# Kernel optimization log

Measured on AMD Instinct MI355X. Metric: run time of the kernel, lower is better.

Reference implementation:

```python
import jax, jax.numpy as jnp
import numpy as np

N_NODES = 20000
N_EDGES = 640000
D = 128


def setup_inputs() -> dict:
    key = jax.random.key(0)
    ks = jax.random.split(key, 8)
    scale = 1.0 / np.sqrt(D)
    x = jax.random.normal(ks[0], (N_NODES, D), dtype=jnp.float32)
    edge_index = jax.random.randint(ks[1], (2, N_EDGES), 0, N_NODES, dtype=jnp.int64)
    W1_rel = jax.random.normal(ks[2], (D, D), dtype=jnp.float32) * scale
    b1_rel = jnp.zeros((D,), dtype=jnp.float32)
    W1_root = jax.random.normal(ks[3], (D, D), dtype=jnp.float32) * scale
    W2_rel = jax.random.normal(ks[4], (D, D), dtype=jnp.float32) * scale
    b2_rel = jnp.zeros((D,), dtype=jnp.float32)
    W2_root = jax.random.normal(ks[5], (D, D), dtype=jnp.float32) * scale
    return {"x": x, "edge_index": edge_index,
            "W1_rel": W1_rel, "b1_rel": b1_rel, "W1_root": W1_root,
            "W2_rel": W2_rel, "b2_rel": b2_rel, "W2_root": W2_root}


def _graph_conv(x, src, dst, W_rel, b_rel, W_root):
    # sum-aggregate neighbor features: gather from src, scatter-add to dst
    agg = jax.ops.segment_sum(x[src], dst, num_segments=N_NODES)  # [N, D]
    # PyG GraphConv: lin_rel(agg) (with bias) + lin_root(x) (no bias)
    return agg @ W_rel + b_rel + x @ W_root


def reference(x, edge_index, W1_rel, b1_rel, W1_root, W2_rel, b2_rel, W2_root):
    src, dst = edge_index[0], edge_index[1]  # messages flow src (j) -> dst (i)
    h = jax.nn.relu(_graph_conv(x, src, dst, W1_rel, b1_rel, W1_root))
    out = _graph_conv(h, src, dst, W2_rel, b2_rel, W2_root)  # final ReLU stripped
    return out
```

## Files before the change

### kernel.cpp

```cpp
#include <hip/hip_runtime.h>

#define N_NODES 20000
#define N_EDGES 640000
#define D 128
#define CAP 128
#define NBINS 157
#define PA_BLOCKS 256
#define EPB 2500
#define SLABCAP 40
#define SRC_SPLIT 10000

typedef __attribute__((ext_vector_type(8))) short bf16x8;
typedef __attribute__((ext_vector_type(4))) float f32x4;

__device__ __forceinline__ short f2bf(float f) {
    union { float f; unsigned u; } un; un.f = f;
    unsigned r = un.u + 0x7fff + ((un.u >> 16) & 1);
    return (short)(r >> 16);
}
__device__ __forceinline__ float bflo(unsigned u) { return __uint_as_float(u << 16); }
__device__ __forceinline__ float bfhi(unsigned u) { return __uint_as_float(u & 0xffff0000u); }

__global__ __launch_bounds__(256) void prep_kernel(
    const float* __restrict__ x,
    const int* __restrict__ src, const int* __restrict__ dst,
    const float* __restrict__ W1_rel, const float* __restrict__ W1_root,
    const float* __restrict__ W2_rel, const float* __restrict__ W2_root,
    unsigned* __restrict__ binned, int* __restrict__ cnts,
    short* __restrict__ xb, short* __restrict__ wpk1, short* __restrict__ wpk2)
{
    const int b = blockIdx.x;
    const int tid = threadIdx.x;
    if (b < PA_BLOCKS) {
        __shared__ int sOff[NBINS];
        for (int i = tid; i < NBINS; i += 256) sOff[i] = 0;
        __syncthreads();
        const int e0 = b * EPB;
        for (int idx = tid; idx < EPB; idx += 256) {
            int d = dst[e0 + idx];
            int s = src[e0 + idx];
            int bin = d >> 7;
            int off = atomicAdd(&sOff[bin], 1);
            if (off < SLABCAP)
                binned[(size_t)(bin * PA_BLOCKS + b) * SLABCAP + off] =
                    ((unsigned)(d & 127) << 16) | (unsigned)s;
        }
        __syncthreads();
        for (int i = tid; i < NBINS; i += 256) {
            int c = sOff[i];
            cnts[i * PA_BLOCKS + b] = (c > SLABCAP) ? SLABCAP : c;
        }
    } else if (b < PA_BLOCKS + 2500) {
        int i = (b - PA_BLOCKS) * 256 + tid;
        float4 v = ((const float4*)x)[i];
        ushort4 o;
        o.x = (unsigned short)f2bf(v.x);
        o.y = (unsigned short)f2bf(v.y);
        o.z = (unsigned short)f2bf(v.z);
        o.w = (unsigned short)f2bf(v.w);
        ((ushort4*)xb)[i] = o;
    } else {
        int pb  = b - (PA_BLOCKS + 2500);
        int job = pb >> 4;
        int idx = (pb & 15) * 256 + tid;
        const float* Wrel  = job ? W2_rel  : W1_rel;
        const float* Wroot = job ? W2_root : W1_root;
        short* Wpk = job ? wpk2 : wpk1;
        int lane = idx & 63;
        int ct   = (idx >> 6) & 7;
        int t    = idx >> 9;
        const float* W = (t < 4) ? Wrel : Wroot;
        int k0  = (t & 3) * 32 + (lane >> 4) * 8;
        int col = ct * 16 + (lane & 15);
        bf16x8 pk;
#pragma unroll
        for (int j = 0; j < 8; j++)
            pk[j] = f2bf(W[(size_t)(k0 + j) * D + col]);
        ((bf16x8*)Wpk)[idx] = pk;
    }
}

__global__ __launch_bounds__(256) void binplace_kernel(
    const unsigned* __restrict__ binned, const int* __restrict__ cnts,
    unsigned short* __restrict__ buckets, int* __restrict__ cnt)
{
    __shared__ int lo[128];
    __shared__ int hi[128];
    const int bin = blockIdx.x;
    const int tid = threadIdx.x;
    if (tid < 128) { lo[tid] = 0; hi[tid] = 0; }
    __syncthreads();
    int c = cnts[bin * PA_BLOCKS + tid];
    const unsigned* rec = binned + (size_t)(bin * PA_BLOCKS + tid) * SLABCAP;
    for (int i = 0; i < c; i++) {
        unsigned u = rec[i];
        int nl = (int)(u >> 16);
        unsigned s = u & 0xffffu;
        if ((int)s < SRC_SPLIT) {
            int slot = atomicAdd(&lo[nl], 1);
            if (slot < CAP)
                buckets[(((bin << 7) | nl) << 7) + slot] = (unsigned short)s;
        } else {
            int slot = CAP - 1 - atomicAdd(&hi[nl], 1);
            if (slot >= 0)
                buckets[(((bin << 7) | nl) << 7) + slot] = (unsigned short)s;
        }
    }
    __syncthreads();
    int node = (bin << 7) + tid;
    if (tid < 128 && node < N_NODES) {
        int nlo = lo[tid]; if (nlo > CAP) nlo = CAP;
        int nhi = hi[tid]; if (nhi > CAP - nlo) nhi = CAP - nlo;
        cnt[node] = nlo | (nhi << 16);
    }
}

__device__ __forceinline__ void gather_range(
    float4& acc, const short* __restrict__ xin,
    uint2 idxpk, int lane, int start, int count)
{
    const int end = start + count;
    int k = start;
    const int full_end = start + (count & ~7);
    for (; k < full_end; k += 8) {
        uint2 u[8];
#pragma unroll
        for (int q = 0; q < 8; q++) {
            int j = k + q;
            unsigned word = __shfl((j & 2) ? idxpk.y : idxpk.x, j >> 2, 32);
            unsigned sidx = (j & 1) ? (word >> 16) : (word & 0xffffu);
            u[q] = *(const uint2*)(xin + (size_t)sidx * D + lane * 4);
        }
#pragma unroll
        for (int q = 0; q < 8; q++) {
            acc.x += bflo(u[q].x); acc.y += bfhi(u[q].x);
            acc.z += bflo(u[q].y); acc.w += bfhi(u[q].y);
        }
    }
    if (k < end) {
        uint2 u[8];
#pragma unroll
        for (int q = 0; q < 8; q++) {
            int j  = k + q;
            int jc = (j < end) ? j : (end - 1);
            unsigned word = __shfl((jc & 2) ? idxpk.y : idxpk.x, jc >> 2, 32);
            unsigned sidx = (jc & 1) ? (word >> 16) : (word & 0xffffu);
            u[q] = *(const uint2*)(xin + (size_t)sidx * D + lane * 4);
        }
#pragma unroll
        for (int q = 0; q < 8; q++) {
            float m = (k + q < end) ? 1.f : 0.f;
            acc.x += m * bflo(u[q].x); acc.y += m * bfhi(u[q].x);
            acc.z += m * bflo(u[q].y); acc.w += m * bfhi(u[q].y);
        }
    }
}

template <bool RELU, bool OUT_BF16>
__global__ __launch_bounds__(512) void layer_kernel(
    const short* __restrict__ xin,
    const int* __restrict__ cnt,
    const unsigned short* __restrict__ buckets,
    const short* __restrict__ Wpk,
    const float* __restrict__ brel,
    void* __restrict__ outp)
{
    __shared__ short sAgg[16][136];

    const int tid  = threadIdx.x;
    const int row0 = blockIdx.x * 16;

    {
        const int hw   = tid >> 5;
        const int lane = tid & 31;
        const int node = row0 + hw;
        int nc  = cnt[node];
        int nlo = nc & 0xffff;
        int nhi = nc >> 16;
        uint2 idxpk = *(const uint2*)(buckets + (node << 7) + lane * 4);

        float4 acc = make_float4(0.f, 0.f, 0.f, 0.f);
        gather_range(acc, xin, idxpk, lane, 0, nlo);
        __syncthreads();
        gather_range(acc, xin, idxpk, lane, CAP - nhi, nhi);

        ushort4 o;
        o.x = (unsigned short)f2bf(acc.x);
        o.y = (unsigned short)f2bf(acc.y);
        o.z = (unsigned short)f2bf(acc.z);
        o.w = (unsigned short)f2bf(acc.w);
        *(ushort4*)&sAgg[hw][lane * 4] = o;
    }
    __syncthreads();

    const int wave = tid >> 6;
    const int lane = tid & 63;
    const int quad = lane >> 4;
    const int l16  = lane & 15;

    f32x4 acc = (f32x4){0.f, 0.f, 0.f, 0.f};
    const short* arow_x = xin + (size_t)(row0 + l16) * D + quad * 8;
    const bf16x8* wb = (const bf16x8*)Wpk + lane;

#pragma unroll
    for (int t = 0; t < 8; t++) {
        bf16x8 a;
        if (t < 4)
            a = *(const bf16x8*)&sAgg[l16][(t & 3) * 32 + quad * 8];
        else
            a = *(const bf16x8*)(arow_x + (t & 3) * 32);
        bf16x8 bfr = wb[(t * 8 + wave) * 64];
        acc = __builtin_amdgcn_mfma_f32_16x16x32_bf16(a, bfr, acc, 0, 0, 0);
    }

    const int col  = wave * 16 + l16;
    const int orow = row0 + quad * 4;
    const float bias = brel[col];
#pragma unroll
    for (int r = 0; r < 4; r++) {
        float v = acc[r] + bias;
        if (RELU) v = fmaxf(v, 0.f);
        if (OUT_BF16)
            ((short*)outp)[(size_t)(orow + r) * D + col] = f2bf(v);
        else
            ((float*)outp)[(size_t)(orow + r) * D + col] = v;
    }
}

extern "C" void kernel_launch(void* const* d_in, const int* in_sizes, int n_in,
                              void* d_out, int out_size, void* d_ws, size_t ws_size,
                              hipStream_t stream) {
    const float* x       = (const float*)d_in[0];
    const int*   ei      = (const int*)  d_in[1];
    const float* W1_rel  = (const float*)d_in[2];
    const float* b1_rel  = (const float*)d_in[3];
    const float* W1_root = (const float*)d_in[4];
    const float* W2_rel  = (const float*)d_in[5];
    const float* b2_rel  = (const float*)d_in[6];
    const float* W2_root = (const float*)d_in[7];
    float* out = (float*)d_out;

    char* p = (char*)d_ws;
    short* xb   = (short*)p;  p += (size_t)N_NODES * D * 2;
    short* hb   = (short*)p;  p += (size_t)N_NODES * D * 2;
    short* wpk1 = (short*)p;  p += 65536;
    short* wpk2 = (short*)p;  p += 65536;
    int*   cnt  = (int*)p;    p += (size_t)N_NODES * 4;
    unsigned short* buckets = (unsigned short*)p;
    p += (size_t)NBINS * 128 * CAP * 2;
    unsigned* binned = (unsigned*)p;
    p += (size_t)NBINS * PA_BLOCKS * SLABCAP * 4;
    int* cnts = (int*)p;

    const int* src = ei;
    const int* dst = ei + N_EDGES;

    prep_kernel<<<PA_BLOCKS + 2500 + 32, 256, 0, stream>>>(
        x, src, dst, W1_rel, W1_root, W2_rel, W2_root,
        binned, cnts, xb, wpk1, wpk2);

    binplace_kernel<<<NBINS, 256, 0, stream>>>(binned, cnts, buckets, cnt);

    layer_kernel<true, true><<<1250, 512, 0, stream>>>(
        xb, cnt, buckets, wpk1, b1_rel, (void*)hb);

    layer_kernel<false, false><<<1250, 512, 0, stream>>>(
        hb, cnt, buckets, wpk2, b2_rel, (void*)out);
}
```

Baseline: 147.8 us.

## Fuse bucket placement into layer kernels with 32-node bins and LDS buckets

Removes the separate binplace kernel and global bucket/count arrays. Each layer block now rebuilds its 32-node CSR-like buckets in shared memory from the per-block binned slabs, then gathers with 16 lanes per node using 16-byte loads and runs two MFMA tiles per wave. This cuts one launch and the global bucket write and read, at the cost of redoing the bucketing in both layers and fewer, larger blocks (625). SLABCAP shrinks to 24, which raises the risk of dropping edges if a bin overflows.

```diff
diff --git a/kernel.cpp b/kernel.cpp
--- a/kernel.cpp
+++ b/kernel.cpp
@@ -4,10 +4,10 @@
 #define N_EDGES 640000
 #define D 128
 #define CAP 128
-#define NBINS 157
+#define NBINS 625
 #define PA_BLOCKS 256
 #define EPB 2500
-#define SLABCAP 40
+#define SLABCAP 24
 #define SRC_SPLIT 10000
 
 typedef __attribute__((ext_vector_type(8))) short bf16x8;
@@ -39,16 +39,16 @@
         for (int idx = tid; idx < EPB; idx += 256) {
             int d = dst[e0 + idx];
             int s = src[e0 + idx];
-            int bin = d >> 7;
+            int bin = d >> 5;
             int off = atomicAdd(&sOff[bin], 1);
             if (off < SLABCAP)
-                binned[(size_t)(bin * PA_BLOCKS + b) * SLABCAP + off] =
-                    ((unsigned)(d & 127) << 16) | (unsigned)s;
+                binned[((size_t)b * NBINS + bin) * SLABCAP + off] =
+                    ((unsigned)(d & 31) << 16) | (unsigned)s;
         }
         __syncthreads();
         for (int i = tid; i < NBINS; i += 256) {
             int c = sOff[i];
-            cnts[i * PA_BLOCKS + b] = (c > SLABCAP) ? SLABCAP : c;
+            cnts[b * NBINS + i] = (c > SLABCAP) ? SLABCAP : c;
         }
     } else if (b < PA_BLOCKS + 2500) {
         int i = (b - PA_BLOCKS) * 256 + tid;
@@ -80,116 +80,103 @@
     }
 }
 
-__global__ __launch_bounds__(256) void binplace_kernel(
-    const unsigned* __restrict__ binned, const int* __restrict__ cnts,
-    unsigned short* __restrict__ buckets, int* __restrict__ cnt)
+__device__ __forceinline__ void gather16(
+    float (&accf)[8], const short* __restrict__ xin,
+    const unsigned short* __restrict__ bkt, int l16, int start, int count)
 {
-    __shared__ int lo[128];
-    __shared__ int hi[128];
-    const int bin = blockIdx.x;
-    const int tid = threadIdx.x;
-    if (tid < 128) { lo[tid] = 0; hi[tid] = 0; }
-    __syncthreads();
-    int c = cnts[bin * PA_BLOCKS + tid];
-    const unsigned* rec = binned + (size_t)(bin * PA_BLOCKS + tid) * SLABCAP;
-    for (int i = 0; i < c; i++) {
-        unsigned u = rec[i];
-        int nl = (int)(u >> 16);
-        unsigned s = u & 0xffffu;
-        if ((int)s < SRC_SPLIT) {
-            int slot = atomicAdd(&lo[nl], 1);
-            if (slot < CAP)
-                buckets[(((bin << 7) | nl) << 7) + slot] = (unsigned short)s;
-        } else {
-            int slot = CAP - 1 - atomicAdd(&hi[nl], 1);
-            if (slot >= 0)
-                buckets[(((bin << 7) | nl) << 7) + slot] = (unsigned short)s;
-        }
-    }
-    __syncthreads();
-    int node = (bin << 7) + tid;
-    if (tid < 128 && node < N_NODES) {
-        int nlo = lo[tid]; if (nlo > CAP) nlo = CAP;
-        int nhi = hi[tid]; if (nhi > CAP - nlo) nhi = CAP - nlo;
-        cnt[node] = nlo | (nhi << 16);
-    }
-}
-
-__device__ __forceinline__ void gather_range(
-    float4& acc, const short* __restrict__ xin,
-    uint2 idxpk, int lane, int start, int count)
-{
-    const int end = start + count;
+    const int end  = start + count;
+    const int fend = start + (count & ~7);
     int k = start;
-    const int full_end = start + (count & ~7);
-    for (; k < full_end; k += 8) {
-        uint2 u[8];
-#pragma unroll
-        for (int q = 0; q < 8; q++) {
-            int j = k + q;
-            unsigned word = __shfl((j & 2) ? idxpk.y : idxpk.x, j >> 2, 32);
-            unsigned sidx = (j & 1) ? (word >> 16) : (word & 0xffffu);
-            u[q] = *(const uint2*)(xin + (size_t)sidx * D + lane * 4);
-        }
-#pragma unroll
-        for (int q = 0; q < 8; q++) {
-            acc.x += bflo(u[q].x); acc.y += bfhi(u[q].x);
-            acc.z += bflo(u[q].y); acc.w += bfhi(u[q].y);
+    for (; k < fend; k += 8) {
+        uint4 u[8];
+#pragma unroll
+        for (int q = 0; q < 8; q++) {
+            unsigned sidx = bkt[k + q];
+            u[q] = *(const uint4*)(xin + (size_t)sidx * D + l16 * 8);
+        }
+#pragma unroll
+        for (int q = 0; q < 8; q++) {
+            accf[0] += bflo(u[q].x); accf[1] += bfhi(u[q].x);
+            accf[2] += bflo(u[q].y); accf[3] += bfhi(u[q].y);
+            accf[4] += bflo(u[q].z); accf[5] += bfhi(u[q].z);
+            accf[6] += bflo(u[q].w); accf[7] += bfhi(u[q].w);
         }
     }
     if (k < end) {
-        uint2 u[8];
+        uint4 u[8];
 #pragma unroll
         for (int q = 0; q < 8; q++) {
             int j  = k + q;
             int jc = (j < end) ? j : (end - 1);
-            unsigned word = __shfl((jc & 2) ? idxpk.y : idxpk.x, jc >> 2, 32);
-            unsigned sidx = (jc & 1) ? (word >> 16) : (word & 0xffffu);
-            u[q] = *(const uint2*)(xin + (size_t)sidx * D + lane * 4);
+            unsigned sidx = bkt[jc];
+            u[q] = *(const uint4*)(xin + (size_t)sidx * D + l16 * 8);
         }
 #pragma unroll
         for (int q = 0; q < 8; q++) {
             float m = (k + q < end) ? 1.f : 0.f;
-            acc.x += m * bflo(u[q].x); acc.y += m * bfhi(u[q].x);
-            acc.z += m * bflo(u[q].y); acc.w += m * bfhi(u[q].y);
+            accf[0] += m * bflo(u[q].x); accf[1] += m * bfhi(u[q].x);
+            accf[2] += m * bflo(u[q].y); accf[3] += m * bfhi(u[q].y);
+            accf[4] += m * bflo(u[q].z); accf[5] += m * bfhi(u[q].z);
+            accf[6] += m * bflo(u[q].w); accf[7] += m * bfhi(u[q].w);
         }
     }
 }
 
 template <bool RELU, bool OUT_BF16>
-__global__ __launch_bounds__(512) void layer_kernel(
+__global__ __launch_bounds__(512, 4) void layer_kernel(
     const short* __restrict__ xin,
-    const int* __restrict__ cnt,
-    const unsigned short* __restrict__ buckets,
+    const unsigned* __restrict__ binned,
+    const int* __restrict__ cnts,
     const short* __restrict__ Wpk,
     const float* __restrict__ brel,
     void* __restrict__ outp)
 {
-    __shared__ short sAgg[16][136];
+    __shared__ unsigned short sBkt[32][CAP + 2];
+    __shared__ short sAgg[32][136];
+    __shared__ int lo[32], hi[32];
 
     const int tid  = threadIdx.x;
-    const int row0 = blockIdx.x * 16;
+    const int g    = blockIdx.x;
+    const int row0 = g * 32;
+
+    if (tid < 32) { lo[tid] = 0; hi[tid] = 0; }
+    __syncthreads();
+    if (tid < PA_BLOCKS) {
+        int c = cnts[tid * NBINS + g];
+        const unsigned* rec = binned + ((size_t)tid * NBINS + g) * SLABCAP;
+        for (int i = 0; i < c; i++) {
+            unsigned u = rec[i];
+            int nl = (int)(u >> 16);
+            unsigned s = u & 0xffffu;
+            if ((int)s < SRC_SPLIT) {
+                int slot = atomicAdd(&lo[nl], 1);
+                if (slot < CAP) sBkt[nl][slot] = (unsigned short)s;
+            } else {
+                int slot = CAP - 1 - atomicAdd(&hi[nl], 1);
+                if (slot >= 0) sBkt[nl][slot] = (unsigned short)s;
+            }
+        }
+    }
+    __syncthreads();
 
     {
-        const int hw   = tid >> 5;
-        const int lane = tid & 31;
-        const int node = row0 + hw;
-        int nc  = cnt[node];
-        int nlo = nc & 0xffff;
-        int nhi = nc >> 16;
-        uint2 idxpk = *(const uint2*)(buckets + (node << 7) + lane * 4);
-
-        float4 acc = make_float4(0.f, 0.f, 0.f, 0.f);
-        gather_range(acc, xin, idxpk, lane, 0, nlo);
+        const int node = tid >> 4;
+        const int l16  = tid & 15;
+        int nlo = lo[node]; if (nlo > CAP) nlo = CAP;
+        int nhi = hi[node]; if (nhi > CAP - nlo) nhi = CAP - nlo;
+
+        float accf[8];
+#pragma unroll
+        for (int j = 0; j < 8; j++) accf[j] = 0.f;
+
+        gather16(accf, xin, sBkt[node], l16, 0, nlo);
         __syncthreads();
-        gather_range(acc, xin, idxpk, lane, CAP - nhi, nhi);
-
-        ushort4 o;
-        o.x = (unsigned short)f2bf(acc.x);
-        o.y = (unsigned short)f2bf(acc.y);
-        o.z = (unsigned short)f2bf(acc.z);
-        o.w = (unsigned short)f2bf(acc.w);
-        *(ushort4*)&sAgg[hw][lane * 4] = o;
+        gather16(accf, xin, sBkt[node], l16, CAP - nhi, nhi);
+
+        bf16x8 pk;
+#pragma unroll
+        for (int j = 0; j < 8; j++) pk[j] = f2bf(accf[j]);
+        *(bf16x8*)&sAgg[node][l16 * 8] = pk;
     }
     __syncthreads();
 
@@ -198,32 +185,43 @@
     const int quad = lane >> 4;
     const int l16  = lane & 15;
 
-    f32x4 acc = (f32x4){0.f, 0.f, 0.f, 0.f};
-    const short* arow_x = xin + (size_t)(row0 + l16) * D + quad * 8;
+    f32x4 acc0 = (f32x4){0.f, 0.f, 0.f, 0.f};
+    f32x4 acc1 = (f32x4){0.f, 0.f, 0.f, 0.f};
+    const short* ax0 = xin + (size_t)(row0 + l16) * D + quad * 8;
+    const short* ax1 = xin + (size_t)(row0 + 16 + l16) * D + quad * 8;
     const bf16x8* wb = (const bf16x8*)Wpk + lane;
 
 #pragma unroll
     for (int t = 0; t < 8; t++) {
-        bf16x8 a;
-        if (t < 4)
-            a = *(const bf16x8*)&sAgg[l16][(t & 3) * 32 + quad * 8];
-        else
-            a = *(const bf16x8*)(arow_x + (t & 3) * 32);
         bf16x8 bfr = wb[(t * 8 + wave) * 64];
-        acc = __builtin_amdgcn_mfma_f32_16x16x32_bf16(a, bfr, acc, 0, 0, 0);
+        bf16x8 a0, a1;
+        if (t < 4) {
+            a0 = *(const bf16x8*)&sAgg[l16][(t & 3) * 32 + quad * 8];
+            a1 = *(const bf16x8*)&sAgg[16 + l16][(t & 3) * 32 + quad * 8];
+        } else {
+            a0 = *(const bf16x8*)(ax0 + (t & 3) * 32);
+            a1 = *(const bf16x8*)(ax1 + (t & 3) * 32);
+        }
+        acc0 = __builtin_amdgcn_mfma_f32_16x16x32_bf16(a0, bfr, acc0, 0, 0, 0);
+        acc1 = __builtin_amdgcn_mfma_f32_16x16x32_bf16(a1, bfr, acc1, 0, 0, 0);
     }
 
     const int col  = wave * 16 + l16;
-    const int orow = row0 + quad * 4;
     const float bias = brel[col];
 #pragma unroll
     for (int r = 0; r < 4; r++) {
-        float v = acc[r] + bias;
-        if (RELU) v = fmaxf(v, 0.f);
-        if (OUT_BF16)
-            ((short*)outp)[(size_t)(orow + r) * D + col] = f2bf(v);
-        else
-            ((float*)outp)[(size_t)(orow + r) * D + col] = v;
+        float v0 = acc0[r] + bias;
+        float v1 = acc1[r] + bias;
+        if (RELU) { v0 = fmaxf(v0, 0.f); v1 = fmaxf(v1, 0.f); }
+        int o0 = row0 + quad * 4 + r;
+        int o1 = o0 + 16;
+        if (OUT_BF16) {
+            ((short*)outp)[(size_t)o0 * D + col] = f2bf(v0);
+            ((short*)outp)[(size_t)o1 * D + col] = f2bf(v1);
+        } else {
+            ((float*)outp)[(size_t)o0 * D + col] = v0;
+            ((float*)outp)[(size_t)o1 * D + col] = v1;
+        }
     }
 }
 
@@ -245,11 +243,8 @@
     short* hb   = (short*)p;  p += (size_t)N_NODES * D * 2;
     short* wpk1 = (short*)p;  p += 65536;
     short* wpk2 = (short*)p;  p += 65536;
-    int*   cnt  = (int*)p;    p += (size_t)N_NODES * 4;
-    unsigned short* buckets = (unsigned short*)p;
-    p += (size_t)NBINS * 128 * CAP * 2;
     unsigned* binned = (unsigned*)p;
-    p += (size_t)NBINS * PA_BLOCKS * SLABCAP * 4;
+    p += (size_t)PA_BLOCKS * NBINS * SLABCAP * 4;
     int* cnts = (int*)p;
 
     const int* src = ei;
@@ -259,11 +254,9 @@
         x, src, dst, W1_rel, W1_root, W2_rel, W2_root,
         binned, cnts, xb, wpk1, wpk2);
 
-    binplace_kernel<<<NBINS, 256, 0, stream>>>(binned, cnts, buckets, cnt);
-
-    layer_kernel<true, true><<<1250, 512, 0, stream>>>(
-        xb, cnt, buckets, wpk1, b1_rel, (void*)hb);
-
-    layer_kernel<false, false><<<1250, 512, 0, stream>>>(
-        hb, cnt, buckets, wpk2, b2_rel, (void*)out);
-}
+    layer_kernel<true, true><<<NBINS, 512, 0, stream>>>(
+        xb, binned, cnts, wpk1, b1_rel, (void*)hb);
+
+    layer_kernel<false, false><<<NBINS, 512, 0, stream>>>(
+        hb, binned, cnts, wpk2, b2_rel, (void*)out);
+}
```

Measured after the change: 150.5 us. Within noise of the previous version (+1.9%).
